# Kernel optimization log

Hardware: AMD Instinct MI355X
Metric: run time of the kernel (lower is better)

## Reference

```python
import jax, jax.numpy as jnp
import numpy as np
from jax import lax

D_MODEL = 1024
D_STATE = 16
D_CONV = 4
EXPAND = 2
DT_RANK = 64
D_INNER = EXPAND * D_MODEL  # 2048
B, L = 2, 2048
LN_EPS = 1e-5


def setup_inputs() -> dict:
    key = jax.random.key(0)
    ks = jax.random.split(key, 8)

    def n(k, shape, s=0.02):
        return jax.random.normal(k, shape, jnp.float32) * s

    # dt_proj bias initialized like mamba_ssm: inverse-softplus of dt in [1e-3, 1e-1]
    dt = jnp.exp(jax.random.uniform(ks[5], (D_INNER,), jnp.float32)
                 * (np.log(0.1) - np.log(0.001)) + np.log(0.001))
    dt_bias = dt + jnp.log(-jnp.expm1(-dt))
    # A_log init: log(1..d_state) per channel (S4D-real init)
    A_init = jnp.tile(jnp.arange(1, D_STATE + 1, dtype=jnp.float32), (D_INNER, 1))

    return {
        "x": jax.random.normal(ks[0], (B, L, D_MODEL), jnp.float32),
        "ln_w": jnp.ones((D_MODEL,), jnp.float32),
        "ln_b": jnp.zeros((D_MODEL,), jnp.float32),
        "in_proj_w": n(ks[1], (2 * D_INNER, D_MODEL)),
        "conv_w": n(ks[2], (D_INNER, D_CONV), 0.1),
        "conv_b": jnp.zeros((D_INNER,), jnp.float32),
        "x_proj_w": n(ks[3], (DT_RANK + 2 * D_STATE, D_INNER)),
        "dt_proj_w": n(ks[4], (D_INNER, DT_RANK), 0.1),
        "dt_proj_b": dt_bias,
        "A_log": jnp.log(A_init),
        "D": jnp.ones((D_INNER,), jnp.float32),
        "out_proj_w": n(ks[6], (D_MODEL, D_INNER)),
    }


def reference(x, ln_w, ln_b, in_proj_w, conv_w, conv_b, x_proj_w,
              dt_proj_w, dt_proj_b, A_log, D, out_proj_w):
    b = x.shape[0]
    # --- pre-norm (LayerNorm) ---
    mu = x.mean(-1, keepdims=True)
    var = jnp.mean(jnp.square(x - mu), axis=-1, keepdims=True)
    xn = (x - mu) * lax.rsqrt(var + LN_EPS) * ln_w + ln_b

    # --- in_proj -> (u, z) ---
    xz = jnp.einsum('bld,ed->ble', xn, in_proj_w)  # (B,L,2*D_INNER)
    u, z = jnp.split(xz, 2, axis=-1)

    # --- causal depthwise conv1d + SiLU ---
    uc = jnp.transpose(u, (0, 2, 1))  # (B, D_INNER, L)
    uc = lax.conv_general_dilated(
        uc, conv_w[:, None, :], window_strides=(1,),
        padding=[(D_CONV - 1, 0)],
        dimension_numbers=('NCH', 'OIH', 'NCH'),
        feature_group_count=D_INNER)
    u = jax.nn.silu(jnp.transpose(uc, (0, 2, 1)) + conv_b)  # (B,L,D_INNER)

    # --- input-dependent dt, B, C ---
    x_dbl = jnp.einsum('bld,ed->ble', u, x_proj_w)  # (B,L,DT_RANK+2*D_STATE)
    dt, Bm, Cm = jnp.split(x_dbl, [DT_RANK, DT_RANK + D_STATE], axis=-1)
    delta = jax.nn.softplus(jnp.einsum('blr,dr->bld', dt, dt_proj_w) + dt_proj_b)

    # --- selective scan ---
    A = -jnp.exp(A_log)  # (D_INNER, D_STATE)
    dA = jnp.exp(jnp.einsum('bld,dn->bldn', delta, A))          # (B,L,D,N)
    dBu = jnp.einsum('bld,bln,bld->bldn', delta, Bm, u)         # (B,L,D,N)

    def step(h, inputs):
        a_t, b_t, c_t = inputs          # (B,D,N), (B,D,N), (B,N)
        h = a_t * h + b_t
        y_t = jnp.einsum('bdn,bn->bd', h, c_t)
        return h, y_t

    h0 = jnp.zeros((b, D_INNER, D_STATE), x.dtype)
    _, ys = lax.scan(step, h0, (dA.transpose(1, 0, 2, 3),
                                dBu.transpose(1, 0, 2, 3),
                                Cm.transpose(1, 0, 2)))  # ys: (L,B,D_INNER)
    y = ys.transpose(1, 0, 2) + u * D  # skip connection via D

    # --- gate + out_proj + residual ---
    y = y * jax.nn.silu(z)
    out = jnp.einsum('bld,ed->ble', y, out_proj_w)
    return out + x
```

## Files before the change

kernel.cpp:

```cpp
#include <hip/hip_runtime.h>
#include <hip/hip_bf16.h>
#include <cstddef>

#define D_MODEL 1024
#define D_STATE 16
#define D_CONV 4
#define DT_RANK 64
#define D_INNER 2048
#define BB 2
#define LL 2048
#define TT (BB * LL)
#define NSEG 64
#define SEGLEN (LL / NSEG)
#define NCHAN (BB * D_INNER)

typedef __bf16 bf16x8 __attribute__((ext_vector_type(8)));
typedef float floatx4 __attribute__((ext_vector_type(4)));

__device__ __forceinline__ unsigned short f2bf(float f) {
  unsigned u = __float_as_uint(f);
  unsigned r = u + 0x7FFF + ((u >> 16) & 1);
  return (unsigned short)(r >> 16);
}
__device__ __forceinline__ float b2f(unsigned short v) {
  return __uint_as_float((unsigned)v << 16);
}

__global__ __launch_bounds__(256) void cast_weights_kernel(
    const float* __restrict__ w0, const float* __restrict__ w1,
    const float* __restrict__ w2, const float* __restrict__ w3,
    unsigned short* __restrict__ dst) {
  int i = blockIdx.x * 256 + threadIdx.x;
  const float* src;
  int off;
  if (i < 1048576) { src = w0; off = 0; }
  else if (i < 1572864) { src = w1; off = 1048576; }
  else if (i < 1622016) { src = w2; off = 1572864; }
  else if (i < 1654784) { src = w3; off = 1622016; }
  else return;
  float4 v = reinterpret_cast<const float4*>(src)[i - off];
  ushort4 o;
  o.x = f2bf(v.x); o.y = f2bf(v.y); o.z = f2bf(v.z); o.w = f2bf(v.w);
  reinterpret_cast<ushort4*>(dst)[i] = o;
}

__global__ __launch_bounds__(256) void cast_dt_kernel(
    const float* __restrict__ xd, unsigned short* __restrict__ dtA) {
  int i = blockIdx.x * 256 + threadIdx.x;
  int row = i >> 4, c = (i & 15) * 4;
  float4 v = *reinterpret_cast<const float4*>(xd + (size_t)row * 96 + c);
  ushort4 o;
  o.x = f2bf(v.x); o.y = f2bf(v.y); o.z = f2bf(v.z); o.w = f2bf(v.w);
  *reinterpret_cast<ushort4*>(dtA + (size_t)row * 64 + c) = o;
}

__global__ __launch_bounds__(256) void layernorm_kernel(
    const float* __restrict__ x, const float* __restrict__ w,
    const float* __restrict__ b, unsigned short* __restrict__ xn) {
  int t = blockIdx.x;
  int tid = threadIdx.x;
  const float4* xr = reinterpret_cast<const float4*>(x + (size_t)t * D_MODEL);
  float4 xv = xr[tid];
  float s = xv.x + xv.y + xv.z + xv.w;
  float sq = xv.x * xv.x + xv.y * xv.y + xv.z * xv.z + xv.w * xv.w;
  for (int off = 32; off >= 1; off >>= 1) {
    s += __shfl_down(s, off);
    sq += __shfl_down(sq, off);
  }
  __shared__ float red[8];
  int wave = tid >> 6;
  if ((tid & 63) == 0) { red[wave * 2] = s; red[wave * 2 + 1] = sq; }
  __syncthreads();
  if (tid == 0) {
    float S = 0.f, Q = 0.f;
    for (int i = 0; i < 4; ++i) { S += red[2 * i]; Q += red[2 * i + 1]; }
    float mean = S * (1.f / D_MODEL);
    float var = Q * (1.f / D_MODEL) - mean * mean;
    red[0] = mean;
    red[1] = rsqrtf(var + 1e-5f);
  }
  __syncthreads();
  float mean = red[0], inv = red[1];
  const float4* wr = reinterpret_cast<const float4*>(w);
  const float4* br = reinterpret_cast<const float4*>(b);
  float4 wv = wr[tid], bv = br[tid];
  ushort4 o;
  o.x = f2bf((xv.x - mean) * inv * wv.x + bv.x);
  o.y = f2bf((xv.y - mean) * inv * wv.y + bv.y);
  o.z = f2bf((xv.z - mean) * inv * wv.z + bv.z);
  o.w = f2bf((xv.w - mean) * inv * wv.w + bv.w);
  reinterpret_cast<ushort4*>(xn + (size_t)t * D_MODEL)[tid] = o;
}

template <int WNF, int EPI, typename OT>
__global__ __launch_bounds__(256) void gemm_bf16_kernel(
    const unsigned short* __restrict__ A, int lda,
    const unsigned short* __restrict__ B, int ldb,
    OT* __restrict__ C, int ldc, int M, int N, int K,
    const float* __restrict__ bias, const float* __restrict__ resid, int ldr,
    unsigned short* __restrict__ C2, int kslice) {
  constexpr int BN = WNF * 32;
  __shared__ unsigned short Atile[128 * 32];
  __shared__ unsigned short Btile[BN * 32];
  const int tid = threadIdx.x;
  const int lane = tid & 63;
  const int wv = tid >> 6;
  const int wrow = (wv >> 1) * 64;
  const int wcol = (wv & 1) * (WNF * 16);
  int gx = gridDim.x, gy = gridDim.y;
  int lid = blockIdx.y * gx + blockIdx.x;
  int rpx = gy >> 3;
  int xcd = lid & 7;
  int q = lid >> 3;
  int by = xcd * rpx + (q % rpx);
  int bx = q / rpx;
  const int row0 = by * 128;
  const int col0 = bx * BN;
  const int m = lane & 15;
  const int qq = lane >> 4;

  int k0lo = 0, k0hi = K;
  if (kslice > 1) {
    int ks = K / kslice;
    k0lo = blockIdx.z * ks;
    k0hi = k0lo + ks;
  }

  floatx4 acc[4][WNF] = {};

  for (int k0 = k0lo; k0 < k0hi; k0 += 32) {
#pragma unroll
    for (int t = 0; t < 2; ++t) {
      int slot = wv * 128 + t * 64 + lane;
      int row = slot >> 2;
      int kg = (slot & 3) ^ ((row >> 1) & 3);
      const unsigned short* ga = A + (size_t)(row0 + row) * lda + k0 + kg * 8;
      __builtin_amdgcn_global_load_lds(
          (const __attribute__((address_space(1))) void*)ga,
          (__attribute__((address_space(3))) void*)(Atile + slot * 8), 16, 0, 0);
    }
#pragma unroll
    for (int t = 0; t < BN / 64; ++t) {
      int slot = (BN == 128) ? (wv * 128 + t * 64 + lane) : tid;
      int row = slot >> 2;
      int kg = (slot & 3) ^ ((row >> 1) & 3);
      int rowB = col0 + row;
      if (rowB >= N) rowB = N - 1;
      const unsigned short* gb = B + (size_t)rowB * ldb + k0 + kg * 8;
      __builtin_amdgcn_global_load_lds(
          (const __attribute__((address_space(1))) void*)gb,
          (__attribute__((address_space(3))) void*)(Btile + slot * 8), 16, 0, 0);
    }
    __syncthreads();
    bf16x8 af[4], bfr[WNF];
#pragma unroll
    for (int i = 0; i < 4; ++i) {
      int ra = wrow + i * 16 + m;
      int sa = ra * 4 + (qq ^ ((ra >> 1) & 3));
      af[i] = *reinterpret_cast<const bf16x8*>(Atile + sa * 8);
    }
#pragma unroll
    for (int j = 0; j < WNF; ++j) {
      int rb = wcol + j * 16 + m;
      int sb = rb * 4 + (qq ^ ((rb >> 1) & 3));
      bfr[j] = *reinterpret_cast<const bf16x8*>(Btile + sb * 8);
    }
#pragma unroll
    for (int i = 0; i < 4; ++i)
#pragma unroll
      for (int j = 0; j < WNF; ++j)
        acc[i][j] = __builtin_amdgcn_mfma_f32_16x16x32_bf16(
            af[i], bfr[j], acc[i][j], 0, 0, 0);
    __syncthreads();
  }

#pragma unroll
  for (int j = 0; j < WNF; ++j) {
    int gc = col0 + wcol + j * 16 + m;
    if (gc >= N) continue;
#pragma unroll
    for (int i = 0; i < 4; ++i) {
#pragma unroll
      for (int r = 0; r < 4; ++r) {
        int gr = row0 + wrow + i * 16 + qq * 4 + r;
        float v = acc[i][j][r];
        if (EPI == 1) {
          float xv = v + bias[gc];
          float sp = fmaxf(xv, 0.f) + log1pf(expf(-fabsf(xv)));
          ((unsigned short*)C)[(size_t)gr * ldc + gc] = f2bf(sp);
        } else if (EPI == 2) {
          ((float*)C)[(size_t)gr * ldc + gc] = v + resid[(size_t)gr * ldr + gc];
        } else if (EPI == 4) {
          if (gc >= D_INNER) {
            float sv = v / (1.f + expf(-v));
            C2[(size_t)gr * D_INNER + (gc - D_INNER)] = f2bf(sv);
          } else {
            ((unsigned short*)C)[(size_t)gr * ldc + gc] = f2bf(v);
          }
        } else {
          if (kslice > 1)
            atomicAdd(&((float*)C)[(size_t)gr * ldc + gc], v);
          else
            ((float*)C)[(size_t)gr * ldc + gc] = v;
        }
      }
    }
  }
}

__global__ __launch_bounds__(256) void conv_silu_kernel(
    const unsigned short* __restrict__ ub, const float* __restrict__ cw,
    const float* __restrict__ cb, unsigned short* __restrict__ ucb) {
  size_t idx = (size_t)blockIdx.x * 256 + threadIdx.x;
  if (idx >= (size_t)TT * D_INNER) return;
  int d = (int)(idx & (D_INNER - 1));
  int t = (int)(idx >> 11);
  int l = t & (LL - 1);
  float acc = cb[d];
#pragma unroll
  for (int k = 0; k < D_CONV; ++k) {
    int ll = l - (D_CONV - 1) + k;
    if (ll >= 0)
      acc += b2f(ub[idx - (size_t)(D_CONV - 1 - k) * D_INNER]) * cw[d * D_CONV + k];
  }
  ucb[idx] = f2bf(acc / (1.f + expf(-acc)));
}

__global__ __launch_bounds__(256) void scan_partial_kernel(
    const unsigned short* __restrict__ deltab, const unsigned short* __restrict__ ucb,
    const float* __restrict__ xd, const float* __restrict__ A_log,
    float* __restrict__ aprod_buf, float* __restrict__ hend_buf) {
  __shared__ float Bs[SEGLEN][16];
  const int tid = threadIdx.x;
  const int d = blockIdx.x * 256 + tid;
  const int s = blockIdx.y;
  const int b = blockIdx.z;
  const int chan = b * D_INNER + d;
  const size_t tbase = (size_t)b * LL + (size_t)s * SEGLEN;

  {
    int row = tid >> 3, pair = tid & 7;
    *reinterpret_cast<float2*>(&Bs[row][pair * 2]) =
        *reinterpret_cast<const float2*>(xd + (tbase + row) * 96 + 64 + pair * 2);
  }
  floatx4 Ac[4];
  {
    const floatx4* ar = reinterpret_cast<const floatx4*>(A_log + (size_t)d * D_STATE);
#pragma unroll
    for (int k = 0; k < 4; ++k) {
      floatx4 v = ar[k];
      for (int j = 0; j < 4; ++j) Ac[k][j] = -__expf(v[j]) * 1.4426950408889634f;
    }
  }
  __syncthreads();

  floatx4 h[4] = {};
  float S = 0.f;
  for (int l = 0; l < SEGLEN; ++l) {
    size_t t = tbase + l;
    float dl = b2f(deltab[t * D_INNER + d]);
    float ul = b2f(ucb[t * D_INNER + d]);
    float dlul = dl * ul;
    S += dl;
#pragma unroll
    for (int k = 0; k < 4; ++k) {
      floatx4 bv = *reinterpret_cast<const floatx4*>(&Bs[l][k * 4]);
      floatx4 a;
      for (int j = 0; j < 4; ++j) a[j] = __builtin_amdgcn_exp2f(dl * Ac[k][j]);
      h[k] = a * h[k] + dlul * bv;
    }
  }
  size_t base = ((size_t)s * NCHAN + chan) * D_STATE;
#pragma unroll
  for (int k = 0; k < 4; ++k) {
    floatx4 ap;
    for (int j = 0; j < 4; ++j) ap[j] = __builtin_amdgcn_exp2f(S * Ac[k][j]);
    *reinterpret_cast<floatx4*>(hend_buf + base + k * 4) = h[k];
    *reinterpret_cast<floatx4*>(aprod_buf + base + k * 4) = ap;
  }
}

__global__ __launch_bounds__(256) void scan_combine_kernel(
    float* __restrict__ aprod_buf, const float* __restrict__ hend_buf) {
  int idx = blockIdx.x * 256 + threadIdx.x;
  float H = 0.f;
  for (int s = 0; s < NSEG; ++s) {
    size_t si = (size_t)s * (NCHAN * D_STATE) + idx;
    float a = aprod_buf[si];
    float he = hend_buf[si];
    aprod_buf[si] = H;
    H = he + a * H;
  }
}

__global__ __launch_bounds__(256) void scan_final_kernel(
    const unsigned short* __restrict__ deltab, const unsigned short* __restrict__ ucb,
    const float* __restrict__ xd, const unsigned short* __restrict__ zsb,
    const float* __restrict__ A_log, const float* __restrict__ Dv,
    const float* __restrict__ hstart_buf, unsigned short* __restrict__ yb) {
  __shared__ float BCs[SEGLEN][32];
  const int tid = threadIdx.x;
  const int d = blockIdx.x * 256 + tid;
  const int s = blockIdx.y;
  const int b = blockIdx.z;
  const int chan = b * D_INNER + d;
  const size_t tbase = (size_t)b * LL + (size_t)s * SEGLEN;

  {
    int row = tid >> 3, quad = tid & 7;
    *reinterpret_cast<float4*>(&BCs[row][quad * 4]) =
        *reinterpret_cast<const float4*>(xd + (tbase + row) * 96 + 64 + quad * 4);
  }
  floatx4 Ac[4];
  {
    const floatx4* ar = reinterpret_cast<const floatx4*>(A_log + (size_t)d * D_STATE);
#pragma unroll
    for (int k = 0; k < 4; ++k) {
      floatx4 v = ar[k];
      for (int j = 0; j < 4; ++j) Ac[k][j] = -__expf(v[j]) * 1.4426950408889634f;
    }
  }
  float Dd = Dv[d];
  floatx4 h[4];
  {
    size_t base = ((size_t)s * NCHAN + chan) * D_STATE;
#pragma unroll
    for (int k = 0; k < 4; ++k)
      h[k] = *reinterpret_cast<const floatx4*>(hstart_buf + base + k * 4);
  }
  __syncthreads();

  for (int l = 0; l < SEGLEN; ++l) {
    size_t t = tbase + l;
    float dl = b2f(deltab[t * D_INNER + d]);
    float ul = b2f(ucb[t * D_INNER + d]);
    float dlul = dl * ul;
    floatx4 psum = {};
#pragma unroll
    for (int k = 0; k < 4; ++k) {
      floatx4 bv = *reinterpret_cast<const floatx4*>(&BCs[l][k * 4]);
      floatx4 cv = *reinterpret_cast<const floatx4*>(&BCs[l][16 + k * 4]);
      floatx4 a;
      for (int j = 0; j < 4; ++j) a[j] = __builtin_amdgcn_exp2f(dl * Ac[k][j]);
      h[k] = a * h[k] + dlul * bv;
      psum += h[k] * cv;
    }
    float p = psum[0] + psum[1] + psum[2] + psum[3];
    float zs = b2f(zsb[t * D_INNER + d]);
    yb[t * D_INNER + d] = f2bf((p + ul * Dd) * zs);
  }
}

extern "C" void kernel_launch(void* const* d_in, const int* in_sizes, int n_in,
                              void* d_out, int out_size, void* d_ws, size_t ws_size,
                              hipStream_t stream) {
  const float* x         = (const float*)d_in[0];
  const float* ln_w      = (const float*)d_in[1];
  const float* ln_b      = (const float*)d_in[2];
  const float* in_proj_w = (const float*)d_in[3];
  const float* conv_w    = (const float*)d_in[4];
  const float* conv_b    = (const float*)d_in[5];
  const float* x_proj_w  = (const float*)d_in[6];
  const float* dt_proj_w = (const float*)d_in[7];
  const float* dt_proj_b = (const float*)d_in[8];
  const float* A_log     = (const float*)d_in[9];
  const float* Dvec      = (const float*)d_in[10];
  const float* out_proj_w= (const float*)d_in[11];
  float* out = (float*)d_out;

  unsigned short* wip = (unsigned short*)d_ws;
  unsigned short* wop = wip + 4194304;
  unsigned short* wxp = wop + 2097152;
  unsigned short* wdt = wxp + 196608;
  unsigned short* xnb = wdt + 131072;
  unsigned short* ub  = xnb + (size_t)TT * D_MODEL;
  unsigned short* ucb = ub + (size_t)TT * D_INNER;
  unsigned short* zsb = ucb + (size_t)TT * D_INNER;
  unsigned short* dtA = zsb + (size_t)TT * D_INNER;
  unsigned short* deltab = dtA + (size_t)TT * DT_RANK;
  float* xd    = (float*)(deltab + (size_t)TT * D_INNER);
  float* hend  = xd + (size_t)TT * 96;
  float* aprod = hend + (size_t)NSEG * NCHAN * D_STATE;

  cast_weights_kernel<<<6464, 256, 0, stream>>>(in_proj_w, out_proj_w,
                                                x_proj_w, dt_proj_w, wip);
  hipMemsetAsync(xd, 0, (size_t)TT * 96 * sizeof(float), stream);

  layernorm_kernel<<<TT, 256, 0, stream>>>(x, ln_w, ln_b, xnb);

  gemm_bf16_kernel<4, 4, unsigned short><<<dim3(32, 32), 256, 0, stream>>>(
      xnb, D_MODEL, wip, D_MODEL, ub, D_INNER, TT, 2 * D_INNER, D_MODEL,
      nullptr, nullptr, 0, zsb, 1);

  conv_silu_kernel<<<(TT * D_INNER) / 256, 256, 0, stream>>>(ub, conv_w, conv_b, ucb);

  gemm_bf16_kernel<2, 0, float><<<dim3(2, 32, 4), 256, 0, stream>>>(
      ucb, D_INNER, wxp, D_INNER, xd, 96, TT, 96, D_INNER,
      nullptr, nullptr, 0, nullptr, 4);

  cast_dt_kernel<<<(TT * DT_RANK / 4) / 256, 256, 0, stream>>>(xd, dtA);
  gemm_bf16_kernel<4, 1, unsigned short><<<dim3(16, 32), 256, 0, stream>>>(
      dtA, DT_RANK, wdt, DT_RANK, deltab, D_INNER, TT, D_INNER, DT_RANK,
      dt_proj_b, nullptr, 0, nullptr, 1);

  scan_partial_kernel<<<dim3(D_INNER / 256, NSEG, BB), 256, 0, stream>>>(
      deltab, ucb, xd, A_log, aprod, hend);
  scan_combine_kernel<<<(NCHAN * D_STATE) / 256, 256, 0, stream>>>(aprod, hend);
  scan_final_kernel<<<dim3(D_INNER / 256, NSEG, BB), 256, 0, stream>>>(
      deltab, ucb, xd, zsb, A_log, Dvec, aprod, ucb);

  gemm_bf16_kernel<2, 2, float><<<dim3(16, 32), 256, 0, stream>>>(
      ucb, D_INNER, wop, D_INNER, out, D_MODEL, TT, D_MODEL, D_INNER,
      nullptr, x, D_MODEL, nullptr, 1);
}
```

Measured before the change: 381.8 us.

## Double GEMM K-tile to 64 and stage bf16 epilogue through LDS

The bf16 MFMA GEMM now loads a K=64 slab per iteration, using an 8-way XOR swizzle, and runs two MFMA sub-steps between barriers. This halves the number of barrier and load rounds per K. The bf16-output epilogues (softplus dt and the in_proj u/z split with SiLU) now write results to shared memory first, then emit coalesced 16-byte row stores instead of scattered 2-byte stores. Shared memory per block grows, which may lower occupancy, and the z-half check now assumes each column tile lies wholly on one side of D_INNER.

```diff
diff --git a/kernel.cpp b/kernel.cpp
--- a/kernel.cpp
+++ b/kernel.cpp
@@ -16,6 +16,7 @@
 
 typedef __bf16 bf16x8 __attribute__((ext_vector_type(8)));
 typedef float floatx4 __attribute__((ext_vector_type(4)));
+typedef unsigned short ushortx8 __attribute__((ext_vector_type(8)));
 
 __device__ __forceinline__ unsigned short f2bf(float f) {
   unsigned u = __float_as_uint(f);
@@ -100,8 +101,15 @@
     const float* __restrict__ bias, const float* __restrict__ resid, int ldr,
     unsigned short* __restrict__ C2, int kslice) {
   constexpr int BN = WNF * 32;
-  __shared__ unsigned short Atile[128 * 32];
-  __shared__ unsigned short Btile[BN * 32];
+  constexpr int BSLOTS = BN * 8;
+  constexpr bool NEEDSTAGE = (EPI == 1 || EPI == 4);
+  constexpr int TILE_USH = 8192 + BN * 64;
+  constexpr int SMEM_USH = NEEDSTAGE && (4 * 64 * 66 > TILE_USH)
+                               ? 4 * 64 * 66 : TILE_USH;
+  __shared__ unsigned short sm[SMEM_USH];
+  unsigned short* Atile = sm;
+  unsigned short* Btile = sm + 8192;
+
   const int tid = threadIdx.x;
   const int lane = tid & 63;
   const int wv = tid >> 6;
@@ -111,13 +119,13 @@
   int lid = blockIdx.y * gx + blockIdx.x;
   int rpx = gy >> 3;
   int xcd = lid & 7;
-  int q = lid >> 3;
-  int by = xcd * rpx + (q % rpx);
-  int bx = q / rpx;
+  int qq0 = lid >> 3;
+  int by = xcd * rpx + (qq0 % rpx);
+  int bx = qq0 / rpx;
   const int row0 = by * 128;
   const int col0 = bx * BN;
   const int m = lane & 15;
-  const int qq = lane >> 4;
+  const int q = lane >> 4;
 
   int k0lo = 0, k0hi = K;
   if (kslice > 1) {
@@ -128,22 +136,22 @@
 
   floatx4 acc[4][WNF] = {};
 
-  for (int k0 = k0lo; k0 < k0hi; k0 += 32) {
-#pragma unroll
-    for (int t = 0; t < 2; ++t) {
-      int slot = wv * 128 + t * 64 + lane;
-      int row = slot >> 2;
-      int kg = (slot & 3) ^ ((row >> 1) & 3);
+  for (int k0 = k0lo; k0 < k0hi; k0 += 64) {
+#pragma unroll
+    for (int t = 0; t < 4; ++t) {
+      int slot = wv * 256 + t * 64 + lane;
+      int row = slot >> 3;
+      int kg = (slot & 7) ^ (row & 7);
       const unsigned short* ga = A + (size_t)(row0 + row) * lda + k0 + kg * 8;
       __builtin_amdgcn_global_load_lds(
           (const __attribute__((address_space(1))) void*)ga,
           (__attribute__((address_space(3))) void*)(Atile + slot * 8), 16, 0, 0);
     }
 #pragma unroll
-    for (int t = 0; t < BN / 64; ++t) {
-      int slot = (BN == 128) ? (wv * 128 + t * 64 + lane) : tid;
-      int row = slot >> 2;
-      int kg = (slot & 3) ^ ((row >> 1) & 3);
+    for (int t = 0; t < BSLOTS / 256; ++t) {
+      int slot = t * 256 + tid;
+      int row = slot >> 3;
+      int kg = (slot & 7) ^ (row & 7);
       int rowB = col0 + row;
       if (rowB >= N) rowB = N - 1;
       const unsigned short* gb = B + (size_t)rowB * ldb + k0 + kg * 8;
@@ -152,56 +160,80 @@
           (__attribute__((address_space(3))) void*)(Btile + slot * 8), 16, 0, 0);
     }
     __syncthreads();
-    bf16x8 af[4], bfr[WNF];
-#pragma unroll
-    for (int i = 0; i < 4; ++i) {
-      int ra = wrow + i * 16 + m;
-      int sa = ra * 4 + (qq ^ ((ra >> 1) & 3));
-      af[i] = *reinterpret_cast<const bf16x8*>(Atile + sa * 8);
-    }
+#pragma unroll
+    for (int s = 0; s < 2; ++s) {
+      int xr = ((s * 4 + q) ^ (m & 7)) * 8;
+      bf16x8 af[4], bfr[WNF];
+#pragma unroll
+      for (int i = 0; i < 4; ++i)
+        af[i] = *reinterpret_cast<const bf16x8*>(
+            Atile + (wrow + i * 16 + m) * 64 + xr);
+#pragma unroll
+      for (int j = 0; j < WNF; ++j)
+        bfr[j] = *reinterpret_cast<const bf16x8*>(
+            Btile + (wcol + j * 16 + m) * 64 + xr);
+#pragma unroll
+      for (int i = 0; i < 4; ++i)
+#pragma unroll
+        for (int j = 0; j < WNF; ++j)
+          acc[i][j] = __builtin_amdgcn_mfma_f32_16x16x32_bf16(
+              af[i], bfr[j], acc[i][j], 0, 0, 0);
+    }
+    __syncthreads();
+  }
+
+  if (NEEDSTAGE) {
+    unsigned short* st = sm + wv * 4224;
+    const bool zhalf = (EPI == 4) && (col0 >= D_INNER);
+#pragma unroll
+    for (int i = 0; i < 4; ++i)
+#pragma unroll
+      for (int j = 0; j < WNF; ++j)
+#pragma unroll
+        for (int r = 0; r < 4; ++r) {
+          float v = acc[i][j][r];
+          if (EPI == 1) {
+            float xv = v + bias[col0 + wcol + j * 16 + m];
+            v = fmaxf(xv, 0.f) + log1pf(expf(-fabsf(xv)));
+          } else if (zhalf) {
+            v = v / (1.f + expf(-v));
+          }
+          st[(i * 16 + q * 4 + r) * 66 + j * 16 + m] = f2bf(v);
+        }
+    __syncthreads();
+    unsigned short* Cb;
+    int cb;
+    if (EPI == 4 && col0 >= D_INNER) { Cb = C2; cb = col0 - D_INNER + wcol; }
+    else { Cb = (unsigned short*)C; cb = col0 + wcol; }
+    constexpr int LPR = WNF * 2;
+    constexpr int RPI = 64 / LPR;
+#pragma unroll
+    for (int t = 0; t < 64 / RPI; ++t) {
+      int r = t * RPI + lane / LPR;
+      int co = (lane % LPR) * 8;
+      ushortx8 val = *reinterpret_cast<const ushortx8*>(st + r * 66 + co);
+      *reinterpret_cast<ushortx8*>(
+          Cb + (size_t)(row0 + wrow + r) * ldc + cb + co) = val;
+    }
+  } else {
 #pragma unroll
     for (int j = 0; j < WNF; ++j) {
-      int rb = wcol + j * 16 + m;
-      int sb = rb * 4 + (qq ^ ((rb >> 1) & 3));
-      bfr[j] = *reinterpret_cast<const bf16x8*>(Btile + sb * 8);
-    }
-#pragma unroll
-    for (int i = 0; i < 4; ++i)
-#pragma unroll
-      for (int j = 0; j < WNF; ++j)
-        acc[i][j] = __builtin_amdgcn_mfma_f32_16x16x32_bf16(
-            af[i], bfr[j], acc[i][j], 0, 0, 0);
-    __syncthreads();
-  }
-
-#pragma unroll
-  for (int j = 0; j < WNF; ++j) {
-    int gc = col0 + wcol + j * 16 + m;
-    if (gc >= N) continue;
-#pragma unroll
-    for (int i = 0; i < 4; ++i) {
-#pragma unroll
-      for (int r = 0; r < 4; ++r) {
-        int gr = row0 + wrow + i * 16 + qq * 4 + r;
-        float v = acc[i][j][r];
-        if (EPI == 1) {
-          float xv = v + bias[gc];
-          float sp = fmaxf(xv, 0.f) + log1pf(expf(-fabsf(xv)));
-          ((unsigned short*)C)[(size_t)gr * ldc + gc] = f2bf(sp);
-        } else if (EPI == 2) {
-          ((float*)C)[(size_t)gr * ldc + gc] = v + resid[(size_t)gr * ldr + gc];
-        } else if (EPI == 4) {
-          if (gc >= D_INNER) {
-            float sv = v / (1.f + expf(-v));
-            C2[(size_t)gr * D_INNER + (gc - D_INNER)] = f2bf(sv);
+      int gc = col0 + wcol + j * 16 + m;
+      if (gc >= N) continue;
+#pragma unroll
+      for (int i = 0; i < 4; ++i) {
+#pragma unroll
+        for (int r = 0; r < 4; ++r) {
+          int gr = row0 + wrow + i * 16 + q * 4 + r;
+          float v = acc[i][j][r];
+          if (EPI == 2) {
+            ((float*)C)[(size_t)gr * ldc + gc] = v + resid[(size_t)gr * ldr + gc];
           } else {
-            ((unsigned short*)C)[(size_t)gr * ldc + gc] = f2bf(v);
+            if (kslice > 1)
+              atomicAdd(&((float*)C)[(size_t)gr * ldc + gc], v);
+            else
+              ((float*)C)[(size_t)gr * ldc + gc] = v;
           }
-        } else {
-          if (kslice > 1)
-            atomicAdd(&((float*)C)[(size_t)gr * ldc + gc], v);
-          else
-            ((float*)C)[(size_t)gr * ldc + gc] = v;
         }
       }
     }
```

New measurement: 362.9 us. 1.05x faster.
